# Kernel tuning notes

Measured on AMD Instinct MI355X. Metric: run time of the kernel, lower is better.

## Reference

```python
import jax, jax.numpy as jnp
import numpy as np

N_NODES = 50000
N_EDGES = 800000
HID = 64
N_LAYERS = 4
POS_DIM = 3
PARAM_SCALE = 0.1
POS_HEAD_SCALE = 0.001  # xavier gain=0.001 on final pos Linear


def setup_inputs() -> dict:
    key = jax.random.key(0)
    ks = jax.random.split(key, 12)
    L, H = N_LAYERS, HID
    s = PARAM_SCALE
    return {
        "x": jax.random.normal(ks[0], (N_NODES, HID), jnp.float32),
        "pos": jax.random.normal(ks[1], (N_NODES, POS_DIM), jnp.float32),
        "edge_index": jax.random.randint(ks[2], (2, N_EDGES), 0, N_NODES, jnp.int32),
        # edge MLP: Linear(2H+1 -> H), SiLU, Linear(H -> H), SiLU
        "We1": jax.random.normal(ks[3], (L, 2 * H + 1, H), jnp.float32) * s,
        "be1": jnp.zeros((L, H), jnp.float32),
        "We2": jax.random.normal(ks[4], (L, H, H), jnp.float32) * s,
        "be2": jnp.zeros((L, H), jnp.float32),
        # node MLP: Linear(2H -> H), SiLU, Linear(H -> H)
        "Wn1": jax.random.normal(ks[5], (L, 2 * H, H), jnp.float32) * s,
        "bn1": jnp.zeros((L, H), jnp.float32),
        "Wn2": jax.random.normal(ks[6], (L, H, H), jnp.float32) * s,
        "bn2": jnp.zeros((L, H), jnp.float32),
        # pos MLP: Linear(H -> H), SiLU, Linear(H -> 1) (tiny init)
        "Wp1": jax.random.normal(ks[7], (L, H, H), jnp.float32) * s,
        "bp1": jnp.zeros((L, H), jnp.float32),
        "Wp2": jax.random.normal(ks[8], (L, H, 1), jnp.float32) * POS_HEAD_SCALE,
        "bp2": jnp.zeros((L, 1), jnp.float32),
        # logit(pos_scale=0.5) == 0
        "pos_scale_logit": jnp.zeros((1,), jnp.float32),
    }


def reference(x, pos, edge_index, We1, be1, We2, be2, Wn1, bn1, Wn2, bn2,
              Wp1, bp1, Wp2, bp2, pos_scale_logit):
    POS_CLAMP = 500.0
    POS_UPDATE_CLAMP = 5.0
    src, dst = edge_index[0], edge_index[1]  # messages flow j=src -> i=dst
    n = x.shape[0]
    L = We1.shape[0]

    # pos is NOT fed back between layers in the torch forward, so edge
    # geometry is constant across layers.
    rel = pos[dst] - pos[src]                     # [E, P]
    d2 = jnp.sum(rel * rel, axis=-1, keepdims=True)  # [E, 1]
    deg = jnp.maximum(
        jax.ops.segment_sum(jnp.ones(src.shape, x.dtype), dst, num_segments=n),
        1.0)[:, None]                             # [N, 1]

    pos_new = pos
    for l in range(L):
        # edge MLP on gathered node pairs
        m = jnp.concatenate([x[dst], x[src], d2], axis=-1)  # [E, 2H+1]
        m = jax.nn.silu(m @ We1[l] + be1[l])
        m = jax.nn.silu(m @ We2[l] + be2[l])                # [E, H]
        # scatter-aggregate messages to target nodes
        agg = jax.ops.segment_sum(m, dst, num_segments=n)   # [N, H]
        # node update MLP
        h = jax.nn.silu(jnp.concatenate([x, agg], axis=-1) @ Wn1[l] + bn1[l])
        x = h @ Wn2[l] + bn2[l]
        # position update: mean over incoming edges of rel * phi_pos(m)
        c = jax.nn.silu(m @ Wp1[l] + bp1[l]) @ Wp2[l] + bp2[l]  # [E, 1]
        pos_new = pos + jax.ops.segment_sum(rel * c, dst, num_segments=n) / deg

    upd = (pos_new - pos) * jax.nn.sigmoid(pos_scale_logit[0])
    upd = jnp.clip(upd, -POS_UPDATE_CLAMP, POS_UPDATE_CLAMP)
    pos_out = jnp.clip(pos + upd, -POS_CLAMP, POS_CLAMP)
    return x, pos_out
```

## Files before the change

kernel.cpp:

```cpp
#include <hip/hip_runtime.h>

#define NN 50000
#define NE 800000
#define TPB 10

typedef __attribute__((ext_vector_type(8))) short short8;
typedef __attribute__((ext_vector_type(4))) float f32x4;

__device__ __forceinline__ float silu_f(float v) {
    return v / (1.0f + __expf(-v));
}
__device__ __forceinline__ unsigned short f2bf(float f) {
    unsigned u = __float_as_uint(f);
    u += 0x7fffu + ((u >> 16) & 1u);
    return (unsigned short)(u >> 16);
}
__device__ __forceinline__ unsigned pk2(float a, float b) {
    return (unsigned)f2bf(a) | ((unsigned)f2bf(b) << 16);
}
__device__ __forceinline__ void gload_lds16(const unsigned short* g, unsigned short* l) {
    __builtin_amdgcn_global_load_lds(
        (const __attribute__((address_space(1))) unsigned int*)g,
        (__attribute__((address_space(3))) unsigned int*)l, 16, 0, 0);
}
#define FENCE_BAR() do { \
    asm volatile("s_waitcnt lgkmcnt(0)" ::: "memory"); \
    __builtin_amdgcn_sched_barrier(0); \
    __builtin_amdgcn_s_barrier(); \
    __builtin_amdgcn_sched_barrier(0); \
} while (0)
#define VMDRAIN() do { \
    __builtin_amdgcn_sched_barrier(0); \
    asm volatile("s_waitcnt vmcnt(0)" ::: "memory"); \
    __builtin_amdgcn_sched_barrier(0); \
} while (0)

__global__ __launch_bounds__(256) void egnn_hist(
    const int* __restrict__ dst, int* __restrict__ hc)
{
    int e = blockIdx.x * 256 + threadIdx.x;
    if (e < NE) atomicAdd(&hc[dst[e]], 1);
}

__global__ __launch_bounds__(1024) void egnn_scan(
    int* __restrict__ hc, int* __restrict__ rowptr)
{
    __shared__ int part[1024];
    const int t = threadIdx.x;
    const int C = (NN + 1023) / 1024;
    const int b0 = t * C;
    int s = 0;
    for (int i = 0; i < C; ++i) {
        int idx = b0 + i;
        if (idx < NN) s += hc[idx];
    }
    part[t] = s;
    __syncthreads();
    for (int off = 1; off < 1024; off <<= 1) {
        int v = (t >= off) ? part[t - off] : 0;
        __syncthreads();
        part[t] += v;
        __syncthreads();
    }
    int run = part[t] - s;
    for (int i = 0; i < C; ++i) {
        int idx = b0 + i;
        if (idx < NN) {
            int v = hc[idx];
            rowptr[idx] = run;
            hc[idx] = run;
            run += v;
        }
    }
    if (t == 1023) rowptr[NN] = part[1023];
}

__global__ __launch_bounds__(256) void egnn_scatter(
    const int* __restrict__ src, const int* __restrict__ dst,
    const float* __restrict__ pos, int* __restrict__ cursor,
    int* __restrict__ eSrc, int* __restrict__ eDst, float* __restrict__ eD2)
{
    int e = blockIdx.x * 256 + threadIdx.x;
    if (e >= NE) return;
    int s = src[e], d = dst[e];
    float rx = pos[3*d+0] - pos[3*s+0];
    float ry = pos[3*d+1] - pos[3*s+1];
    float rz = pos[3*d+2] - pos[3*s+2];
    int p = atomicAdd(&cursor[d], 1);
    eSrc[p] = s;
    eDst[p] = d;
    eD2[p]  = rx*rx + ry*ry + rz*rz;
}

__global__ __launch_bounds__(256) void egnn_prep_w(
    const float* __restrict__ We1, const float* __restrict__ We2,
    unsigned short* __restrict__ Wg1, unsigned short* __restrict__ Wg2)
{
    int i = blockIdx.x * 256 + threadIdx.x;
    if (i < 4 * 64 * 128) {
        int k = i & 127, n = (i >> 7) & 63, l = i >> 13;
        Wg1[(size_t)(l * 64 + n) * 136 + k] = f2bf(We1[((size_t)l * 129 + k) * 64 + n]);
    }
    if (i < 4 * 64 * 64) {
        int h = i & 63, n = (i >> 6) & 63, l = i >> 12;
        Wg2[(size_t)(l * 64 + n) * 72 + h] = f2bf(We2[((size_t)l * 64 + h) * 64 + n]);
    }
}

__global__ __launch_bounds__(256) void egnn_xbf(
    const float* __restrict__ x, unsigned short* __restrict__ xbf)
{
    int i = blockIdx.x * 256 + threadIdx.x;
    if (i >= NN * 16) return;
    float4 v = ((const float4*)x)[i];
    ((uint2*)xbf)[i] = make_uint2(pk2(v.x, v.y), pk2(v.z, v.w));
}

template<bool POS>
__global__ __launch_bounds__(256) void egnn_edge(
    const unsigned short* __restrict__ xbf, const float* __restrict__ eD2,
    const int* __restrict__ eSrc, const int* __restrict__ eDst,
    const float* __restrict__ pos,
    const unsigned short* __restrict__ Wg1, const unsigned short* __restrict__ Wg2,
    const float* __restrict__ We1,
    const float* __restrict__ be1, const float* __restrict__ be2,
    const float* __restrict__ Wp1, const float* __restrict__ bp1,
    const float* __restrict__ Wp2, const float* __restrict__ bp2,
    float* __restrict__ agg, float* __restrict__ dpos, int layer)
{
    __shared__ __align__(16) unsigned char pool[16384 * 2 + 16640];
    __shared__ int   sS[2][64];
    __shared__ int   sD[2][64];
    __shared__ float s2[2][64];
    __shared__ float sC[64];

    unsigned short* const xls0 = (unsigned short*)pool;
    unsigned short* const xls1 = (unsigned short*)(pool + 16384);
    unsigned short* const m1l  = (unsigned short*)(pool + 32768);
    float* const          sM2f = (float*)(pool + 32768);

    const int t    = threadIdx.x;
    const int lane = t & 63;
    const int w    = t >> 6;
    const int l15  = lane & 15;
    const int g    = lane >> 4;
    const int eh   = w >> 1;
    const int ch   = w & 1;
    const int er   = lane >> 4;
    const int half = (lane >> 3) & 1;
    const int c    = lane & 7;
    const int tile0 = blockIdx.x * TPB;

    const unsigned short* W1b = &Wg1[(size_t)(layer * 64) * 136];
    const unsigned short* W2b = &Wg2[(size_t)(layer * 64) * 72];
    short8 w1f0[4], w1f1[4], w2f0[2], w2f1[2];
    #pragma unroll
    for (int ks = 0; ks < 4; ++ks) {
        w1f0[ks] = *(const short8*)&W1b[(ch * 32 +      l15) * 136 + ks * 32 + g * 8];
        w1f1[ks] = *(const short8*)&W1b[(ch * 32 + 16 + l15) * 136 + ks * 32 + g * 8];
    }
    #pragma unroll
    for (int ks = 0; ks < 2; ++ks) {
        w2f0[ks] = *(const short8*)&W2b[(ch * 32 +      l15) * 72 + ks * 32 + g * 8];
        w2f1[ks] = *(const short8*)&W2b[(ch * 32 + 16 + l15) * 72 + ks * 32 + g * 8];
    }
    float4 wrv[2], b1v[2], b2v[2];
    {
        const float* Wr = &We1[((size_t)layer * 129 + 128) * 64];
        const float* B1 = &be1[layer * 64];
        const float* B2 = &be2[layer * 64];
        #pragma unroll
        for (int nt = 0; nt < 2; ++nt) {
            int n0 = ch * 32 + nt * 16 + g * 4;
            wrv[nt] = *(const float4*)&Wr[n0];
            b1v[nt] = *(const float4*)&B1[n0];
            b2v[nt] = *(const float4*)&B2[n0];
        }
    }

    const int* const ip = half ? eSrc : eDst;
    const int ebase = w * 16 + er;

    int nid[4];
    {
        const int gb0 = tile0 * 64;
        #pragma unroll
        for (int i = 0; i < 4; ++i) nid[i] = ip[gb0 + ebase + i * 4];
        #pragma unroll
        for (int i = 0; i < 4; ++i)
            gload_lds16(&xbf[(size_t)nid[i] * 64 + ((c ^ ((ebase + i * 4) & 7)) << 3)],
                        xls0 + w * 2048 + i * 512);
        __builtin_amdgcn_sched_barrier(0);
        #pragma unroll
        for (int i = 0; i < 4; ++i) nid[i] = ip[gb0 + 64 + ebase + i * 4];
        if (t < 64) { sS[0][t] = eSrc[gb0 + t]; sD[0][t] = eDst[gb0 + t]; s2[0][t] = eD2[gb0 + t]; }
    }
    int stS = 0, stD = 0; float st2 = 0.f;
    if (t < 64) {
        const int gb1 = (tile0 + 1) * 64;
        stS = eSrc[gb1 + t]; stD = eDst[gb1 + t]; st2 = eD2[gb1 + t];
    }
    float bp2v = 0.f;
    if (POS) { bp2v = bp2[layer]; if (t < 64) sC[t] = bp2v; }
    VMDRAIN();
    FENCE_BAR();

    const f32x4 zero = {0.f, 0.f, 0.f, 0.f};

    for (int tt = 0; tt < TPB; ++tt) {
        const int b = tt & 1;
        unsigned short* const xcur = b ? xls1 : xls0;
        unsigned short* const xnxt = b ? xls0 : xls1;

        if (tt + 1 < TPB) {
            #pragma unroll
            for (int i = 0; i < 4; ++i)
                gload_lds16(&xbf[(size_t)nid[i] * 64 + ((c ^ ((ebase + i * 4) & 7)) << 3)],
                            xnxt + w * 2048 + i * 512);
            __builtin_amdgcn_sched_barrier(0);
            if (tt + 2 < TPB) {
                const int gb2 = (tile0 + tt + 2) * 64;
                #pragma unroll
                for (int i = 0; i < 4; ++i) nid[i] = ip[gb2 + ebase + i * 4];
            }
        }

        f32x4 a00 = zero, a01 = zero, a10 = zero, a11 = zero;
        {
            const int r0 = (eh * 32 + l15) * 128;
            const int r1 = r0 + 16 * 128;
            const int r7 = l15 & 7;
            #pragma unroll
            for (int ks = 0; ks < 4; ++ks) {
                int col = (((ks << 2) + g) ^ r7) << 3;
                short8 fb0 = *(const short8*)&xcur[r0 + col];
                short8 fb1 = *(const short8*)&xcur[r1 + col];
                a00 = __builtin_amdgcn_mfma_f32_16x16x32_bf16(w1f0[ks], fb0, a00, 0, 0, 0);
                a01 = __builtin_amdgcn_mfma_f32_16x16x32_bf16(w1f0[ks], fb1, a01, 0, 0, 0);
                a10 = __builtin_amdgcn_mfma_f32_16x16x32_bf16(w1f1[ks], fb0, a10, 0, 0, 0);
                a11 = __builtin_amdgcn_mfma_f32_16x16x32_bf16(w1f1[ks], fb1, a11, 0, 0, 0);
            }
        }
        {
            float d2e0 = s2[b][eh * 32 + l15];
            float d2e1 = s2[b][eh * 32 + 16 + l15];
            int e0 = eh * 32 + l15;
            int e1 = e0 + 16;
            #pragma unroll
            for (int nt = 0; nt < 2; ++nt) {
                int n0 = ch * 32 + nt * 16 + g * 4;
                float4 wr = wrv[nt], bb = b1v[nt];
                f32x4 acc0 = nt ? a10 : a00;
                f32x4 acc1 = nt ? a11 : a01;
                float r0 = silu_f(acc0.x + d2e0 * wr.x + bb.x);
                float r1 = silu_f(acc0.y + d2e0 * wr.y + bb.y);
                float r2 = silu_f(acc0.z + d2e0 * wr.z + bb.z);
                float r3 = silu_f(acc0.w + d2e0 * wr.w + bb.w);
                *(uint2*)&m1l[e0 * 72 + n0] = make_uint2(pk2(r0, r1), pk2(r2, r3));
                r0 = silu_f(acc1.x + d2e1 * wr.x + bb.x);
                r1 = silu_f(acc1.y + d2e1 * wr.y + bb.y);
                r2 = silu_f(acc1.z + d2e1 * wr.z + bb.z);
                r3 = silu_f(acc1.w + d2e1 * wr.w + bb.w);
                *(uint2*)&m1l[e1 * 72 + n0] = make_uint2(pk2(r0, r1), pk2(r2, r3));
            }
        }
        FENCE_BAR();

        f32x4 c00 = zero, c01 = zero, c10 = zero, c11 = zero;
        #pragma unroll
        for (int ks = 0; ks < 2; ++ks) {
            short8 fb0 = *(const short8*)&m1l[(eh * 32 +      l15) * 72 + ks * 32 + g * 8];
            short8 fb1 = *(const short8*)&m1l[(eh * 32 + 16 + l15) * 72 + ks * 32 + g * 8];
            c00 = __builtin_amdgcn_mfma_f32_16x16x32_bf16(w2f0[ks], fb0, c00, 0, 0, 0);
            c01 = __builtin_amdgcn_mfma_f32_16x16x32_bf16(w2f0[ks], fb1, c01, 0, 0, 0);
            c10 = __builtin_amdgcn_mfma_f32_16x16x32_bf16(w2f1[ks], fb0, c10, 0, 0, 0);
            c11 = __builtin_amdgcn_mfma_f32_16x16x32_bf16(w2f1[ks], fb1, c11, 0, 0, 0);
        }
        FENCE_BAR();

        {
            int e0 = eh * 32 + l15;
            int e1 = e0 + 16;
            #pragma unroll
            for (int nt = 0; nt < 2; ++nt) {
                int n0 = ch * 32 + nt * 16 + g * 4;
                float4 bb = b2v[nt];
                f32x4 acc0 = nt ? c10 : c00;
                f32x4 acc1 = nt ? c11 : c01;
                sM2f[e0 * 65 + n0 + 0] = silu_f(acc0.x + bb.x);
                sM2f[e0 * 65 + n0 + 1] = silu_f(acc0.y + bb.y);
                sM2f[e0 * 65 + n0 + 2] = silu_f(acc0.z + bb.z);
                sM2f[e0 * 65 + n0 + 3] = silu_f(acc0.w + bb.w);
                sM2f[e1 * 65 + n0 + 0] = silu_f(acc1.x + bb.x);
                sM2f[e1 * 65 + n0 + 1] = silu_f(acc1.y + bb.y);
                sM2f[e1 * 65 + n0 + 2] = silu_f(acc1.z + bb.z);
                sM2f[e1 * 65 + n0 + 3] = silu_f(acc1.w + bb.w);
            }
        }
        if (tt + 1 < TPB && t < 64) {
            sS[1 - b][t] = stS; sD[1 - b][t] = stD; s2[1 - b][t] = st2;
            if (tt + 2 < TPB) {
                const int gb2 = (tile0 + tt + 2) * 64;
                stS = eSrc[gb2 + t]; stD = eDst[gb2 + t]; st2 = eD2[gb2 + t];
            }
        }
        FENCE_BAR();

        if (POS) {
            const int wofs = __builtin_amdgcn_readfirstlane(w * 16);
            float p1[16];
            {
                const float* bP1 = &bp1[(size_t)layer * 64 + wofs];
                #pragma unroll
                for (int hh = 0; hh < 16; ++hh) p1[hh] = bP1[hh];
            }
            const float* P1 = &Wp1[(size_t)layer * 64 * 64 + wofs];
            for (int k = 0; k < 64; ++k) {
                float mv = sM2f[lane * 65 + k];
                const float* wr2 = P1 + k * 64;
                #pragma unroll
                for (int hh = 0; hh < 16; ++hh) p1[hh] = fmaf(mv, wr2[hh], p1[hh]);
            }
            float part = 0.0f;
            {
                const float* P2 = &Wp2[(size_t)layer * 64 + wofs];
                #pragma unroll
                for (int hh = 0; hh < 16; ++hh) part += silu_f(p1[hh]) * P2[hh];
            }
            atomicAdd(&sC[lane], part);
            FENCE_BAR();
            if (w == 0) {
                float cc = sC[lane];
                int d = sD[b][lane], s = sS[b][lane];
                float rx = pos[3*d+0] - pos[3*s+0];
                float ry = pos[3*d+1] - pos[3*s+1];
                float rz = pos[3*d+2] - pos[3*s+2];
                atomicAdd(&dpos[3*(size_t)d+0], rx * cc);
                atomicAdd(&dpos[3*(size_t)d+1], ry * cc);
                atomicAdd(&dpos[3*(size_t)d+2], rz * cc);
            }
            FENCE_BAR();
            if (t < 64) sC[t] = bp2v;
        }

        VMDRAIN();

        {
            const int e0 = w * 16;
            float v[16];
            #pragma unroll
            for (int i = 0; i < 16; ++i) v[i] = sM2f[(e0 + i) * 65 + lane];
            int dd[16];
            #pragma unroll
            for (int i = 0; i < 16; ++i) dd[i] = sD[b][e0 + i];
            float run = v[0];
            int cur = dd[0];
            #pragma unroll
            for (int i = 1; i < 16; ++i) {
                if (dd[i] != cur) {
                    atomicAdd(&agg[(size_t)cur * 64 + lane], run);
                    run = 0.0f;
                    cur = dd[i];
                }
                run += v[i];
            }
            atomicAdd(&agg[(size_t)cur * 64 + lane], run);
        }
        FENCE_BAR();
    }
}

__global__ __launch_bounds__(256) void egnn_node(
    const float* __restrict__ x, const float* __restrict__ agg,
    const float* __restrict__ Wn1, const float* __restrict__ bn1,
    const float* __restrict__ Wn2, const float* __restrict__ bn2,
    float* __restrict__ xout, unsigned short* __restrict__ xbf_out, int layer)
{
    __shared__ float sX[64 * 65];
    __shared__ float sA[64 * 65];

    const int t    = threadIdx.x;
    const int w    = t >> 6;
    const int lane = t & 63;
    const int base = blockIdx.x * 64;
    const int nval = (NN - base < 64) ? (NN - base) : 64;
    const int wofs = __builtin_amdgcn_readfirstlane(w * 16);

    #pragma unroll
    for (int i = 0; i < 4; ++i) {
        int idx = i * 256 + t;
        int e = idx >> 4, c = idx & 15;
        if (e < nval) {
            const float4 vx = *reinterpret_cast<const float4*>(&x[(size_t)(base + e) * 64 + c * 4]);
            const float4 va = *reinterpret_cast<const float4*>(&agg[(size_t)(base + e) * 64 + c * 4]);
            float* px = &sX[e * 65 + c * 4];
            float* pa = &sA[e * 65 + c * 4];
            px[0]=vx.x; px[1]=vx.y; px[2]=vx.z; px[3]=vx.w;
            pa[0]=va.x; pa[1]=va.y; pa[2]=va.z; pa[3]=va.w;
        }
    }
    __syncthreads();

    float acc[16];
    {
        const float* b = &bn1[(size_t)layer * 64 + wofs];
        #pragma unroll
        for (int hh = 0; hh < 16; ++hh) acc[hh] = b[hh];
    }
    const float* W1 = &Wn1[(size_t)layer * 128 * 64 + wofs];
    for (int k = 0; k < 64; ++k) {
        float inv = sX[lane * 65 + k];
        const float* wr = W1 + k * 64;
        #pragma unroll
        for (int hh = 0; hh < 16; ++hh) acc[hh] = fmaf(inv, wr[hh], acc[hh]);
    }
    for (int k = 0; k < 64; ++k) {
        float inv = sA[lane * 65 + k];
        const float* wr = W1 + (64 + k) * 64;
        #pragma unroll
        for (int hh = 0; hh < 16; ++hh) acc[hh] = fmaf(inv, wr[hh], acc[hh]);
    }
    #pragma unroll
    for (int hh = 0; hh < 16; ++hh) acc[hh] = silu_f(acc[hh]);
    __syncthreads();
    #pragma unroll
    for (int hh = 0; hh < 16; ++hh) sA[lane * 65 + wofs + hh] = acc[hh];
    __syncthreads();

    float o[16];
    {
        const float* b = &bn2[(size_t)layer * 64 + wofs];
        #pragma unroll
        for (int hh = 0; hh < 16; ++hh) o[hh] = b[hh];
    }
    const float* W2 = &Wn2[(size_t)layer * 64 * 64 + wofs];
    for (int k = 0; k < 64; ++k) {
        float inv = sA[lane * 65 + k];
        const float* wr = W2 + k * 64;
        #pragma unroll
        for (int hh = 0; hh < 16; ++hh) o[hh] = fmaf(inv, wr[hh], o[hh]);
    }
    if (lane < nval) {
        uint4 u0, u1;
        u0.x = pk2(o[0], o[1]);   u0.y = pk2(o[2],  o[3]);
        u0.z = pk2(o[4], o[5]);   u0.w = pk2(o[6],  o[7]);
        u1.x = pk2(o[8], o[9]);   u1.y = pk2(o[10], o[11]);
        u1.z = pk2(o[12], o[13]); u1.w = pk2(o[14], o[15]);
        *(uint4*)&xbf_out[(size_t)(base + lane) * 64 + wofs + 0] = u0;
        *(uint4*)&xbf_out[(size_t)(base + lane) * 64 + wofs + 8] = u1;
    }
    #pragma unroll
    for (int hh = 0; hh < 16; ++hh) sX[lane * 65 + wofs + hh] = o[hh];
    __syncthreads();
    #pragma unroll
    for (int i = 0; i < 4; ++i) {
        int idx = i * 256 + t;
        int e = idx >> 4, c = idx & 15;
        if (e < nval) {
            float4 v;
            const float* p = &sX[e * 65 + c * 4];
            v.x = p[0]; v.y = p[1]; v.z = p[2]; v.w = p[3];
            *reinterpret_cast<float4*>(&xout[(size_t)(base + e) * 64 + c * 4]) = v;
        }
    }
}

__global__ __launch_bounds__(256) void egnn_final(
    const float* __restrict__ pos, const float* __restrict__ dpos,
    const int* __restrict__ rowptr, const float* __restrict__ logit,
    float* __restrict__ pos_out)
{
    int i = blockIdx.x * 256 + threadIdx.x;
    if (i >= NN * 3) return;
    int node = i / 3;
    float dg = fmaxf((float)(rowptr[node + 1] - rowptr[node]), 1.0f);
    float sig = 1.0f / (1.0f + __expf(-logit[0]));
    float upd = (dpos[i] / dg) * sig;
    upd = fminf(fmaxf(upd, -5.0f), 5.0f);
    float p = pos[i] + upd;
    pos_out[i] = fminf(fmaxf(p, -500.0f), 500.0f);
}

extern "C" void kernel_launch(void* const* d_in, const int* in_sizes, int n_in,
                              void* d_out, int out_size, void* d_ws, size_t ws_size,
                              hipStream_t stream)
{
    const float* x0    = (const float*)d_in[0];
    const float* pos   = (const float*)d_in[1];
    const int*   src   = (const int*)d_in[2];
    const int*   dst   = src + NE;
    const float* We1   = (const float*)d_in[3];
    const float* be1   = (const float*)d_in[4];
    const float* We2   = (const float*)d_in[5];
    const float* be2   = (const float*)d_in[6];
    const float* Wn1   = (const float*)d_in[7];
    const float* bn1   = (const float*)d_in[8];
    const float* Wn2   = (const float*)d_in[9];
    const float* bn2   = (const float*)d_in[10];
    const float* Wp1   = (const float*)d_in[11];
    const float* bp1   = (const float*)d_in[12];
    const float* Wp2   = (const float*)d_in[13];
    const float* bp2   = (const float*)d_in[14];
    const float* logit = (const float*)d_in[15];

    float* xout    = (float*)d_out;
    float* pos_out = xout + (size_t)NN * 64;

    float* ws  = (float*)d_ws;
    float* xA   = ws;  ws += (size_t)NN * 64;
    float* agg  = ws;  ws += (size_t)NN * 64;
    float* dpos = ws;  ws += (size_t)NN * 3;
    float* eD2  = ws;  ws += NE;
    int* rowptr = (int*)ws;  ws += NN + 1;
    int* hc     = (int*)ws;  ws += NN;
    int* eSrc   = (int*)ws;  ws += NE;
    int* eDst   = (int*)ws;  ws += NE;
    unsigned short* xbf = (unsigned short*)ws;
    ws += (size_t)NN * 32;
    unsigned short* Wg1 = (unsigned short*)ws;
    unsigned short* Wg2 = Wg1 + 4 * 64 * 136;

    hipMemsetAsync(hc, 0, NN * sizeof(int), stream);
    hipMemsetAsync(dpos, 0, (size_t)NN * 3 * sizeof(float), stream);
    egnn_hist<<<NE / 256, 256, 0, stream>>>(dst, hc);
    egnn_scan<<<1, 1024, 0, stream>>>(hc, rowptr);
    egnn_scatter<<<NE / 256, 256, 0, stream>>>(src, dst, pos, hc, eSrc, eDst, eD2);
    egnn_prep_w<<<128, 256, 0, stream>>>(We1, We2, Wg1, Wg2);
    egnn_xbf<<<(NN * 16 + 255) / 256, 256, 0, stream>>>(x0, xbf);

    const int nblk = NE / 64 / TPB;
    const float* xin = x0;
    for (int l = 0; l < 4; ++l) {
        hipMemsetAsync(agg, 0, (size_t)NN * 64 * sizeof(float), stream);
        if (l == 3) {
            egnn_edge<true><<<nblk, 256, 0, stream>>>(
                xbf, eD2, eSrc, eDst, pos, Wg1, Wg2, We1, be1, be2,
                Wp1, bp1, Wp2, bp2, agg, dpos, l);
        } else {
            egnn_edge<false><<<nblk, 256, 0, stream>>>(
                xbf, eD2, eSrc, eDst, pos, Wg1, Wg2, We1, be1, be2,
                Wp1, bp1, Wp2, bp2, agg, dpos, l);
        }
        float* xo = (l % 2 == 0) ? xA : xout;
        egnn_node<<<(NN + 63) / 64, 256, 0, stream>>>(xin, agg, Wn1, bn1, Wn2, bn2, xo, xbf, l);
        xin = xo;
    }
    egnn_final<<<(NN * 3 + 255) / 256, 256, 0, stream>>>(pos, dpos, rowptr, logit, pos_out);
}
```

Measured before the change: 967.0 us.

## Move node MLP to bf16 MFMA and rebalance edge tiles per block

Replaces the scalar fp32 node-update MLP with a bf16 MFMA kernel. The kernel reads node features from the bf16 copy already kept for the edge kernel and converts agg to bf16 in shared memory. Node weights are pre-packed to bf16 once. The fp32 x output is written only on the last layer, which drops the ping-pong fp32 buffer. Separately, the edge kernel processes 17 tiles per block with a tail guard instead of 10, cutting block count and per-block weight-load overhead. The trade-off is that x inputs to the node MLP lose precision relative to fp32.

```diff
diff --git a/kernel.cpp b/kernel.cpp
--- a/kernel.cpp
+++ b/kernel.cpp
@@ -2,7 +2,8 @@
 
 #define NN 50000
 #define NE 800000
-#define TPB 10
+#define NTILES 12500
+#define TPB 17
 
 typedef __attribute__((ext_vector_type(8))) short short8;
 typedef __attribute__((ext_vector_type(4))) float f32x4;
@@ -107,6 +108,21 @@
     }
 }
 
+__global__ __launch_bounds__(256) void egnn_prep_wn(
+    const float* __restrict__ Wn1, const float* __restrict__ Wn2,
+    unsigned short* __restrict__ Wgn1, unsigned short* __restrict__ Wgn2)
+{
+    int i = blockIdx.x * 256 + threadIdx.x;
+    if (i < 4 * 64 * 128) {
+        int k = i & 127, n = (i >> 7) & 63, l = i >> 13;
+        Wgn1[(size_t)(l * 64 + n) * 136 + k] = f2bf(Wn1[((size_t)l * 128 + k) * 64 + n]);
+    }
+    if (i < 4 * 64 * 64) {
+        int h = i & 63, n = (i >> 6) & 63, l = i >> 12;
+        Wgn2[(size_t)(l * 64 + n) * 72 + h] = f2bf(Wn2[((size_t)l * 64 + h) * 64 + n]);
+    }
+}
+
 __global__ __launch_bounds__(256) void egnn_xbf(
     const float* __restrict__ x, unsigned short* __restrict__ xbf)
 {
@@ -150,6 +166,7 @@
     const int half = (lane >> 3) & 1;
     const int c    = lane & 7;
     const int tile0 = blockIdx.x * TPB;
+    const int ntiles = (NTILES - tile0 < TPB) ? (NTILES - tile0) : TPB;
 
     const unsigned short* W1b = &Wg1[(size_t)(layer * 64) * 136];
     const unsigned short* W2b = &Wg2[(size_t)(layer * 64) * 72];
@@ -191,12 +208,14 @@
             gload_lds16(&xbf[(size_t)nid[i] * 64 + ((c ^ ((ebase + i * 4) & 7)) << 3)],
                         xls0 + w * 2048 + i * 512);
         __builtin_amdgcn_sched_barrier(0);
-        #pragma unroll
-        for (int i = 0; i < 4; ++i) nid[i] = ip[gb0 + 64 + ebase + i * 4];
+        if (ntiles > 1) {
+            #pragma unroll
+            for (int i = 0; i < 4; ++i) nid[i] = ip[gb0 + 64 + ebase + i * 4];
+        }
         if (t < 64) { sS[0][t] = eSrc[gb0 + t]; sD[0][t] = eDst[gb0 + t]; s2[0][t] = eD2[gb0 + t]; }
     }
     int stS = 0, stD = 0; float st2 = 0.f;
-    if (t < 64) {
+    if (ntiles > 1 && t < 64) {
         const int gb1 = (tile0 + 1) * 64;
         stS = eSrc[gb1 + t]; stD = eDst[gb1 + t]; st2 = eD2[gb1 + t];
     }
@@ -207,18 +226,18 @@
 
     const f32x4 zero = {0.f, 0.f, 0.f, 0.f};
 
-    for (int tt = 0; tt < TPB; ++tt) {
+    for (int tt = 0; tt < ntiles; ++tt) {
         const int b = tt & 1;
         unsigned short* const xcur = b ? xls1 : xls0;
         unsigned short* const xnxt = b ? xls0 : xls1;
 
-        if (tt + 1 < TPB) {
+        if (tt + 1 < ntiles) {
             #pragma unroll
             for (int i = 0; i < 4; ++i)
                 gload_lds16(&xbf[(size_t)nid[i] * 64 + ((c ^ ((ebase + i * 4) & 7)) << 3)],
                             xnxt + w * 2048 + i * 512);
             __builtin_amdgcn_sched_barrier(0);
-            if (tt + 2 < TPB) {
+            if (tt + 2 < ntiles) {
                 const int gb2 = (tile0 + tt + 2) * 64;
                 #pragma unroll
                 for (int i = 0; i < 4; ++i) nid[i] = ip[gb2 + ebase + i * 4];
@@ -297,9 +316,9 @@
                 sM2f[e1 * 65 + n0 + 3] = silu_f(acc1.w + bb.w);
             }
         }
-        if (tt + 1 < TPB && t < 64) {
+        if (tt + 1 < ntiles && t < 64) {
             sS[1 - b][t] = stS; sD[1 - b][t] = stD; s2[1 - b][t] = st2;
-            if (tt + 2 < TPB) {
+            if (tt + 2 < ntiles) {
                 const int gb2 = (tile0 + tt + 2) * 64;
                 stS = eSrc[gb2 + t]; stD = eDst[gb2 + t]; st2 = eD2[gb2 + t];
             }
@@ -370,97 +389,176 @@
     }
 }
 
-__global__ __launch_bounds__(256) void egnn_node(
-    const float* __restrict__ x, const float* __restrict__ agg,
-    const float* __restrict__ Wn1, const float* __restrict__ bn1,
-    const float* __restrict__ Wn2, const float* __restrict__ bn2,
+template<bool WRITE_F32>
+__global__ __launch_bounds__(256) void egnn_node_mfma(
+    const unsigned short* __restrict__ xbf, const float* __restrict__ agg,
+    const unsigned short* __restrict__ Wgn1, const unsigned short* __restrict__ Wgn2,
+    const float* __restrict__ bn1, const float* __restrict__ bn2,
     float* __restrict__ xout, unsigned short* __restrict__ xbf_out, int layer)
 {
-    __shared__ float sX[64 * 65];
-    __shared__ float sA[64 * 65];
+    __shared__ __align__(16) unsigned char pool[16384 + 9216];
+    unsigned short* const xpl = (unsigned short*)pool;
+    unsigned short* const m1l = (unsigned short*)(pool + 16384);
+    float* const          sXf = (float*)pool;
 
     const int t    = threadIdx.x;
+    const int lane = t & 63;
     const int w    = t >> 6;
-    const int lane = t & 63;
+    const int l15  = lane & 15;
+    const int g    = lane >> 4;
+    const int eh   = w >> 1;
+    const int ch   = w & 1;
     const int base = blockIdx.x * 64;
     const int nval = (NN - base < 64) ? (NN - base) : 64;
-    const int wofs = __builtin_amdgcn_readfirstlane(w * 16);
 
     #pragma unroll
-    for (int i = 0; i < 4; ++i) {
-        int idx = i * 256 + t;
-        int e = idx >> 4, c = idx & 15;
+    for (int i = 0; i < 2; ++i) {
+        int e = w * 16 + i * 8 + (lane >> 3);
+        int node = base + ((e < nval) ? e : 0);
+        gload_lds16(&xbf[(size_t)node * 64 + (((lane & 7) ^ (e & 7)) << 3)],
+                    xpl + w * 1024 + i * 512);
+    }
+    __builtin_amdgcn_sched_barrier(0);
+
+    const unsigned short* W1b = &Wgn1[(size_t)(layer * 64) * 136];
+    const unsigned short* W2b = &Wgn2[(size_t)(layer * 64) * 72];
+    short8 w1f0[4], w1f1[4], w2f0[2], w2f1[2];
+    #pragma unroll
+    for (int ks = 0; ks < 4; ++ks) {
+        w1f0[ks] = *(const short8*)&W1b[(ch * 32 +      l15) * 136 + ks * 32 + g * 8];
+        w1f1[ks] = *(const short8*)&W1b[(ch * 32 + 16 + l15) * 136 + ks * 32 + g * 8];
+    }
+    #pragma unroll
+    for (int ks = 0; ks < 2; ++ks) {
+        w2f0[ks] = *(const short8*)&W2b[(ch * 32 +      l15) * 72 + ks * 32 + g * 8];
+        w2f1[ks] = *(const short8*)&W2b[(ch * 32 + 16 + l15) * 72 + ks * 32 + g * 8];
+    }
+    float4 b1v[2], b2v[2];
+    {
+        const float* B1 = &bn1[layer * 64];
+        const float* B2 = &bn2[layer * 64];
+        #pragma unroll
+        for (int nt = 0; nt < 2; ++nt) {
+            int n0 = ch * 32 + nt * 16 + g * 4;
+            b1v[nt] = *(const float4*)&B1[n0];
+            b2v[nt] = *(const float4*)&B2[n0];
+        }
+    }
+
+    {
+        int e = t >> 2, q = t & 3;
+        int node = base + ((e < nval) ? e : 0);
+        const float4* ap = (const float4*)&agg[(size_t)node * 64 + q * 16];
+        float4 v0 = ap[0], v1 = ap[1], v2 = ap[2], v3 = ap[3];
+        uint4 u0, u1;
+        u0.x = pk2(v0.x, v0.y); u0.y = pk2(v0.z, v0.w);
+        u0.z = pk2(v1.x, v1.y); u0.w = pk2(v1.z, v1.w);
+        u1.x = pk2(v2.x, v2.y); u1.y = pk2(v2.z, v2.w);
+        u1.z = pk2(v3.x, v3.y); u1.w = pk2(v3.z, v3.w);
+        *(uint4*)&xpl[4096 + e * 64 + (((2 * q)     ^ (e & 7)) << 3)] = u0;
+        *(uint4*)&xpl[4096 + e * 64 + (((2 * q + 1) ^ (e & 7)) << 3)] = u1;
+    }
+    __syncthreads();
+
+    const f32x4 zero = {0.f, 0.f, 0.f, 0.f};
+    f32x4 a00 = zero, a01 = zero, a10 = zero, a11 = zero;
+    {
+        const int e0 = eh * 32 + l15;
+        const int e1 = e0 + 16;
+        const int r7 = e0 & 7;
+        #pragma unroll
+        for (int ks = 0; ks < 4; ++ks) {
+            int kc = (ks << 2) + g;
+            int off0 = (kc >> 3) * 4096 + e0 * 64 + (((kc & 7) ^ r7) << 3);
+            int off1 = (kc >> 3) * 4096 + e1 * 64 + (((kc & 7) ^ r7) << 3);
+            short8 fb0 = *(const short8*)&xpl[off0];
+            short8 fb1 = *(const short8*)&xpl[off1];
+            a00 = __builtin_amdgcn_mfma_f32_16x16x32_bf16(w1f0[ks], fb0, a00, 0, 0, 0);
+            a01 = __builtin_amdgcn_mfma_f32_16x16x32_bf16(w1f0[ks], fb1, a01, 0, 0, 0);
+            a10 = __builtin_amdgcn_mfma_f32_16x16x32_bf16(w1f1[ks], fb0, a10, 0, 0, 0);
+            a11 = __builtin_amdgcn_mfma_f32_16x16x32_bf16(w1f1[ks], fb1, a11, 0, 0, 0);
+        }
+    }
+    {
+        int e0 = eh * 32 + l15;
+        int e1 = e0 + 16;
+        #pragma unroll
+        for (int nt = 0; nt < 2; ++nt) {
+            int n0 = ch * 32 + nt * 16 + g * 4;
+            float4 bb = b1v[nt];
+            f32x4 acc0 = nt ? a10 : a00;
+            f32x4 acc1 = nt ? a11 : a01;
+            float r0 = silu_f(acc0.x + bb.x);
+            float r1 = silu_f(acc0.y + bb.y);
+            float r2 = silu_f(acc0.z + bb.z);
+            float r3 = silu_f(acc0.w + bb.w);
+            *(uint2*)&m1l[e0 * 72 + n0] = make_uint2(pk2(r0, r1), pk2(r2, r3));
+            r0 = silu_f(acc1.x + bb.x);
+            r1 = silu_f(acc1.y + bb.y);
+            r2 = silu_f(acc1.z + bb.z);
+            r3 = silu_f(acc1.w + bb.w);
+            *(uint2*)&m1l[e1 * 72 + n0] = make_uint2(pk2(r0, r1), pk2(r2, r3));
+        }
+    }
+    __syncthreads();
+
+    f32x4 c00 = zero, c01 = zero, c10 = zero, c11 = zero;
+    #pragma unroll
+    for (int ks = 0; ks < 2; ++ks) {
+        short8 fb0 = *(const short8*)&m1l[(eh * 32 +      l15) * 72 + ks * 32 + g * 8];
+        short8 fb1 = *(const short8*)&m1l[(eh * 32 + 16 + l15) * 72 + ks * 32 + g * 8];
+        c00 = __builtin_amdgcn_mfma_f32_16x16x32_bf16(w2f0[ks], fb0, c00, 0, 0, 0);
+        c01 = __builtin_amdgcn_mfma_f32_16x16x32_bf16(w2f0[ks], fb1, c01, 0, 0, 0);
+        c10 = __builtin_amdgcn_mfma_f32_16x16x32_bf16(w2f1[ks], fb0, c10, 0, 0, 0);
+        c11 = __builtin_amdgcn_mfma_f32_16x16x32_bf16(w2f1[ks], fb1, c11, 0, 0, 0);
+    }
+    __syncthreads();
+
+    {
+        int e0 = eh * 32 + l15;
+        int e1 = e0 + 16;
+        #pragma unroll
+        for (int nt = 0; nt < 2; ++nt) {
+            int n0 = ch * 32 + nt * 16 + g * 4;
+            float4 bb = b2v[nt];
+            f32x4 acc0 = nt ? c10 : c00;
+            f32x4 acc1 = nt ? c11 : c01;
+            sXf[e0 * 65 + n0 + 0] = acc0.x + bb.x;
+            sXf[e0 * 65 + n0 + 1] = acc0.y + bb.y;
+            sXf[e0 * 65 + n0 + 2] = acc0.z + bb.z;
+            sXf[e0 * 65 + n0 + 3] = acc0.w + bb.w;
+            sXf[e1 * 65 + n0 + 0] = acc1.x + bb.x;
+            sXf[e1 * 65 + n0 + 1] = acc1.y + bb.y;
+            sXf[e1 * 65 + n0 + 2] = acc1.z + bb.z;
+            sXf[e1 * 65 + n0 + 3] = acc1.w + bb.w;
+        }
+    }
+    __syncthreads();
+
+    if (WRITE_F32) {
+        #pragma unroll
+        for (int i = 0; i < 4; ++i) {
+            int idx = i * 256 + t;
+            int e = idx >> 4, c = idx & 15;
+            if (e < nval) {
+                float4 v;
+                const float* p = &sXf[e * 65 + c * 4];
+                v.x = p[0]; v.y = p[1]; v.z = p[2]; v.w = p[3];
+                *reinterpret_cast<float4*>(&xout[(size_t)(base + e) * 64 + c * 4]) = v;
+            }
+        }
+    }
+    {
+        int e = t >> 2, q = t & 3;
         if (e < nval) {
-            const float4 vx = *reinterpret_cast<const float4*>(&x[(size_t)(base + e) * 64 + c * 4]);
-            const float4 va = *reinterpret_cast<const float4*>(&agg[(size_t)(base + e) * 64 + c * 4]);
-            float* px = &sX[e * 65 + c * 4];
-            float* pa = &sA[e * 65 + c * 4];
-            px[0]=vx.x; px[1]=vx.y; px[2]=vx.z; px[3]=vx.w;
-            pa[0]=va.x; pa[1]=va.y; pa[2]=va.z; pa[3]=va.w;
-        }
-    }
-    __syncthreads();
-
-    float acc[16];
-    {
-        const float* b = &bn1[(size_t)layer * 64 + wofs];
-        #pragma unroll
-        for (int hh = 0; hh < 16; ++hh) acc[hh] = b[hh];
-    }
-    const float* W1 = &Wn1[(size_t)layer * 128 * 64 + wofs];
-    for (int k = 0; k < 64; ++k) {
-        float inv = sX[lane * 65 + k];
-        const float* wr = W1 + k * 64;
-        #pragma unroll
-        for (int hh = 0; hh < 16; ++hh) acc[hh] = fmaf(inv, wr[hh], acc[hh]);
-    }
-    for (int k = 0; k < 64; ++k) {
-        float inv = sA[lane * 65 + k];
-        const float* wr = W1 + (64 + k) * 64;
-        #pragma unroll
-        for (int hh = 0; hh < 16; ++hh) acc[hh] = fmaf(inv, wr[hh], acc[hh]);
-    }
-    #pragma unroll
-    for (int hh = 0; hh < 16; ++hh) acc[hh] = silu_f(acc[hh]);
-    __syncthreads();
-    #pragma unroll
-    for (int hh = 0; hh < 16; ++hh) sA[lane * 65 + wofs + hh] = acc[hh];
-    __syncthreads();
-
-    float o[16];
-    {
-        const float* b = &bn2[(size_t)layer * 64 + wofs];
-        #pragma unroll
-        for (int hh = 0; hh < 16; ++hh) o[hh] = b[hh];
-    }
-    const float* W2 = &Wn2[(size_t)layer * 64 * 64 + wofs];
-    for (int k = 0; k < 64; ++k) {
-        float inv = sA[lane * 65 + k];
-        const float* wr = W2 + k * 64;
-        #pragma unroll
-        for (int hh = 0; hh < 16; ++hh) o[hh] = fmaf(inv, wr[hh], o[hh]);
-    }
-    if (lane < nval) {
-        uint4 u0, u1;
-        u0.x = pk2(o[0], o[1]);   u0.y = pk2(o[2],  o[3]);
-        u0.z = pk2(o[4], o[5]);   u0.w = pk2(o[6],  o[7]);
-        u1.x = pk2(o[8], o[9]);   u1.y = pk2(o[10], o[11]);
-        u1.z = pk2(o[12], o[13]); u1.w = pk2(o[14], o[15]);
-        *(uint4*)&xbf_out[(size_t)(base + lane) * 64 + wofs + 0] = u0;
-        *(uint4*)&xbf_out[(size_t)(base + lane) * 64 + wofs + 8] = u1;
-    }
-    #pragma unroll
-    for (int hh = 0; hh < 16; ++hh) sX[lane * 65 + wofs + hh] = o[hh];
-    __syncthreads();
-    #pragma unroll
-    for (int i = 0; i < 4; ++i) {
-        int idx = i * 256 + t;
-        int e = idx >> 4, c = idx & 15;
-        if (e < nval) {
-            float4 v;
-            const float* p = &sX[e * 65 + c * 4];
-            v.x = p[0]; v.y = p[1]; v.z = p[2]; v.w = p[3];
-            *reinterpret_cast<float4*>(&xout[(size_t)(base + e) * 64 + c * 4]) = v;
+            const float* p = &sXf[e * 65 + q * 16];
+            uint4 u0, u1;
+            u0.x = pk2(p[0],  p[1]);  u0.y = pk2(p[2],  p[3]);
+            u0.z = pk2(p[4],  p[5]);  u0.w = pk2(p[6],  p[7]);
+            u1.x = pk2(p[8],  p[9]);  u1.y = pk2(p[10], p[11]);
+            u1.z = pk2(p[12], p[13]); u1.w = pk2(p[14], p[15]);
+            *(uint4*)&xbf_out[(size_t)(base + e) * 64 + q * 16 + 0] = u0;
+            *(uint4*)&xbf_out[(size_t)(base + e) * 64 + q * 16 + 8] = u1;
         }
     }
 }
@@ -507,7 +605,6 @@
     float* pos_out = xout + (size_t)NN * 64;
 
     float* ws  = (float*)d_ws;
-    float* xA   = ws;  ws += (size_t)NN * 64;
     float* agg  = ws;  ws += (size_t)NN * 64;
     float* dpos = ws;  ws += (size_t)NN * 3;
     float* eD2  = ws;  ws += NE;
@@ -517,8 +614,10 @@
     int* eDst   = (int*)ws;  ws += NE;
     unsigned short* xbf = (unsigned short*)ws;
     ws += (size_t)NN * 32;
-    unsigned short* Wg1 = (unsigned short*)ws;
-    unsigned short* Wg2 = Wg1 + 4 * 64 * 136;
+    unsigned short* Wg1  = (unsigned short*)ws;
+    unsigned short* Wg2  = Wg1 + 4 * 64 * 136;
+    unsigned short* Wgn1 = Wg2 + 4 * 64 * 72;
+    unsigned short* Wgn2 = Wgn1 + 4 * 64 * 136;
 
     hipMemsetAsync(hc, 0, NN * sizeof(int), stream);
     hipMemsetAsync(dpos, 0, (size_t)NN * 3 * sizeof(float), stream);
@@ -526,24 +625,26 @@
     egnn_scan<<<1, 1024, 0, stream>>>(hc, rowptr);
     egnn_scatter<<<NE / 256, 256, 0, stream>>>(src, dst, pos, hc, eSrc, eDst, eD2);
     egnn_prep_w<<<128, 256, 0, stream>>>(We1, We2, Wg1, Wg2);
+    egnn_prep_wn<<<128, 256, 0, stream>>>(Wn1, Wn2, Wgn1, Wgn2);
     egnn_xbf<<<(NN * 16 + 255) / 256, 256, 0, stream>>>(x0, xbf);
 
-    const int nblk = NE / 64 / TPB;
-    const float* xin = x0;
+    const int nblk = (NTILES + TPB - 1) / TPB;
+    const int nodeblk = (NN + 63) / 64;
     for (int l = 0; l < 4; ++l) {
         hipMemsetAsync(agg, 0, (size_t)NN * 64 * sizeof(float), stream);
         if (l == 3) {
             egnn_edge<true><<<nblk, 256, 0, stream>>>(
                 xbf, eD2, eSrc, eDst, pos, Wg1, Wg2, We1, be1, be2,
                 Wp1, bp1, Wp2, bp2, agg, dpos, l);
+            egnn_node_mfma<true><<<nodeblk, 256, 0, stream>>>(
+                xbf, agg, Wgn1, Wgn2, bn1, bn2, xout, xbf, l);
         } else {
             egnn_edge<false><<<nblk, 256, 0, stream>>>(
                 xbf, eD2, eSrc, eDst, pos, Wg1, Wg2, We1, be1, be2,
                 Wp1, bp1, Wp2, bp2, agg, dpos, l);
-        }
-        float* xo = (l % 2 == 0) ? xA : xout;
-        egnn_node<<<(NN + 63) / 64, 256, 0, stream>>>(xin, agg, Wn1, bn1, Wn2, bn2, xo, xbf, l);
-        xin = xo;
+            egnn_node_mfma<false><<<nodeblk, 256, 0, stream>>>(
+                xbf, agg, Wgn1, Wgn2, bn1, bn2, xout, xbf, l);
+        }
     }
     egnn_final<<<(NN * 3 + 255) / 256, 256, 0, stream>>>(pos, dpos, rowptr, logit, pos_out);
 }
```

Measured after the change: 991.2 us. +2.5%, slower.
